# Kernel optimization log

Hardware: AMD Instinct MI355X
Metric: run time of the kernel (lower is better)

## Reference

```python
import jax, jax.numpy as jnp
import numpy as np
from jax import lax

B, T = 128, 128
MODEL = 128          # model_size = hidden_size = cell_size (w)
R = 4                # read heads
M = 64               # nr_cells
W = MODEL            # cell size
VOCAB = 512
CLIP = 20.0          # dnc default controller clip
DELTA = 1e-6         # dnc epsilon
IFACE = R * W + 3 * W + 5 * R + 3  # 919 interface outputs


def setup_inputs():
    key = jax.random.key(0)
    ks = jax.random.split(key, 12)
    g = lambda k, s, sc: jax.random.normal(k, s, dtype=jnp.float32) * sc
    H = MODEL
    return {
        'tokens': jax.random.randint(ks[0], (B, T), 0, VOCAB),
        'emb': g(ks[1], (VOCAB, MODEL), 0.02),
        # controller: 2-layer LSTM, layer0 input = model + r*w
        'w_ih0': g(ks[2], (4 * H, MODEL + R * W), 0.05),
        'w_hh0': g(ks[3], (4 * H, H), 0.05),
        'b_ih0': jnp.zeros((4 * H,), jnp.float32),
        'b_hh0': jnp.zeros((4 * H,), jnp.float32),
        'w_ih1': g(ks[4], (4 * H, H), 0.05),
        'w_hh1': g(ks[5], (4 * H, H), 0.05),
        'b_ih1': jnp.zeros((4 * H,), jnp.float32),
        'b_hh1': jnp.zeros((4 * H,), jnp.float32),
        # memory interface linear: hidden -> 919
        'w_iface': g(ks[6], (IFACE, H), 0.05),
        'b_iface': jnp.zeros((IFACE,), jnp.float32),
        # dnc output linear: (hidden + r*w) -> model
        'w_out': g(ks[7], (MODEL, H + R * W), 0.05),
        'b_out': jnp.zeros((MODEL,), jnp.float32),
        # DNCAE fc head: model -> vocab
        'w_fc': g(ks[8], (VOCAB, MODEL), 0.05),
        'b_fc': jnp.zeros((VOCAB,), jnp.float32),
        # dnc initializes controller h (and c = h.clone()) with xavier-uniform noise
        'h0': g(ks[9], (2, B, H), 0.1),
    }


def _lstm_step(x, h, c, w_ih, w_hh, b_ih, b_hh):
    gates = x @ w_ih.T + b_ih + h @ w_hh.T + b_hh
    i, f, g, o = jnp.split(gates, 4, axis=-1)  # pytorch gate order i,f,g,o
    c2 = jax.nn.sigmoid(f) * c + jax.nn.sigmoid(i) * jnp.tanh(g)
    h2 = jax.nn.sigmoid(o) * jnp.tanh(c2)
    return h2, c2


def _cosine(mem, keys):
    # mem (B,M,W), keys (B,K,W) -> similarity (B,K,M); dnc adds DELTA to norms
    mn = mem / (jnp.linalg.norm(mem, axis=2, keepdims=True) + DELTA)
    kn = keys / (jnp.linalg.norm(keys, axis=2, keepdims=True) + DELTA)
    return jnp.einsum('bmw,bkw->bkm', mn, kn)


def _dnc_forward(tokens, emb, w_ih0, w_hh0, b_ih0, b_hh0, w_ih1, w_hh1, b_ih1,
                 b_hh1, w_iface, b_iface, w_out, b_out, w_fc, b_fc, h0):
    x = emb[tokens]  # (B,T,MODEL)
    # ixaxaar dnc concatenates the *initial* last_read (zeros) to every timestep input
    xs = jnp.concatenate([x, jnp.zeros((B, T, R * W), x.dtype)], axis=-1)
    eye_mask = 1.0 - jnp.eye(M, dtype=x.dtype)

    def step(carry, x_t):
        hl0, hl1, cl0, cl1, mem, link, prec, rw, ww, usage = carry
        nh0, nc0 = _lstm_step(x_t, hl0, cl0, w_ih0, w_hh0, b_ih0, b_hh0)
        nh1, nc1 = _lstm_step(nh0, hl1, cl1, w_ih1, w_hh1, b_ih1, b_hh1)
        out = jnp.clip(nh1, -CLIP, CLIP)
        xi = out @ w_iface.T + b_iface  # (B, 919)
        o = R * W
        read_keys = jnp.tanh(xi[:, :R * W]).reshape(B, R, W)
        read_str = jax.nn.softplus(xi[:, o:o + R]); o += R
        write_key = jnp.tanh(xi[:, o:o + W]).reshape(B, 1, W); o += W
        write_str = jax.nn.softplus(xi[:, o:o + 1]); o += 1
        erase = jax.nn.sigmoid(xi[:, o:o + W]); o += W
        write_vec = jnp.tanh(xi[:, o:o + W]); o += W
        free_gates = jax.nn.sigmoid(xi[:, o:o + R]); o += R
        alloc_gate = jax.nn.sigmoid(xi[:, o:o + 1]); o += 1
        write_gate = jax.nn.sigmoid(xi[:, o:o + 1]); o += 1
        read_modes = jax.nn.softmax(xi[:, o:o + 3 * R].reshape(B, R, 3), axis=2)

        # ---- write phase ----
        # usage (single write head: 1-prod(1-ww) == ww)
        usage = usage + (1.0 - usage) * ww
        psi = jnp.prod(1.0 - free_gates[:, :, None] * rw, axis=1)  # (B,M)
        usage = usage * psi
        # content weighting on pre-write memory
        wcw = jax.nn.softmax(_cosine(mem, write_key) * write_str[:, :, None], axis=2)[:, 0, :]
        # allocation weighting via sorted-usage cumprod
        u = DELTA + (1.0 - DELTA) * usage
        phi = jnp.argsort(u, axis=1)
        sorted_u = jnp.take_along_axis(u, phi, axis=1)
        prod_su = jnp.cumprod(jnp.concatenate([jnp.ones((B, 1), u.dtype), sorted_u], axis=1), axis=1)[:, :-1]
        sorted_alloc = (1.0 - sorted_u) * prod_su
        alloc = jnp.take_along_axis(sorted_alloc, jnp.argsort(phi, axis=1), axis=1)
        # final write weighting (B,M)
        ww = write_gate * (alloc_gate * alloc + (1.0 - alloc_gate) * wcw)
        # erase + write memory
        mem = mem * (1.0 - ww[:, :, None] * erase[:, None, :]) + ww[:, :, None] * write_vec[:, None, :]
        # temporal link matrix
        ww_i = ww[:, :, None]
        ww_j = ww[:, None, :]
        link = (1.0 - ww_i - ww_j) * link + ww_i * prec[:, None, :]
        link = link * eye_mask
        prec = (1.0 - jnp.sum(ww, axis=1, keepdims=True)) * prec + ww

        # ---- read phase (on post-write memory) ----
        cw = jax.nn.softmax(_cosine(mem, read_keys) * read_str[:, :, None], axis=2)  # (B,R,M)
        fwd = jnp.einsum('bij,brj->bri', link, rw)
        bwd = jnp.einsum('bri,bij->brj', rw, link)
        rw = read_modes[:, :, 0:1] * bwd + read_modes[:, :, 1:2] * fwd + read_modes[:, :, 2:3] * cw
        read_vecs = jnp.einsum('brm,bmw->brw', rw, mem).reshape(B, R * W)

        y = jnp.concatenate([out, read_vecs], axis=-1) @ w_out.T + b_out  # (B,MODEL)
        return (nh0, nh1, nc0, nc1, mem, link, prec, rw, ww, usage), y

    z = jnp.zeros
    carry0 = (h0[0], h0[1], h0[0], h0[1],
              z((B, M, W), jnp.float32), z((B, M, M), jnp.float32), z((B, M), jnp.float32),
              z((B, R, M), jnp.float32), z((B, M), jnp.float32), z((B, M), jnp.float32))
    _, ys = lax.scan(step, carry0, jnp.swapaxes(xs, 0, 1))  # ys (T,B,MODEL)
    dnc_out = jnp.swapaxes(ys, 0, 1)  # (B,T,MODEL)
    logits = dnc_out @ w_fc.T + b_fc  # (B,T,VOCAB)
    return jnp.transpose(logits, (0, 2, 1))  # (B,VOCAB,T) like .permute(0,2,1)


def reference(tokens, emb, w_ih0, w_hh0, b_ih0, b_hh0, w_ih1, w_hh1, b_ih1,
              b_hh1, w_iface, b_iface, w_out, b_out, w_fc, b_fc, h0):
    return _dnc_forward(tokens, emb, w_ih0, w_hh0, b_ih0, b_hh0, w_ih1, w_hh1,
                        b_ih1, b_hh1, w_iface, b_iface, w_out, b_out, w_fc, b_fc, h0)
```

## Files before the change

### kernel.cpp

```cpp
#include <hip/hip_runtime.h>
#include <math.h>

#define B 128
#define T 128
#define H 128
#define RH 4
#define M 64
#define W 128
#define VOCAB 512
#define IFACE 919
#define G4 512
#define DELTA 1e-6f
#define CLIPV 20.0f

#define MEMLD 133
#define LNKLD 67
#define CH 8
#define XILD 928

__device__ __forceinline__ float sigmoidf_(float x){ return 1.0f/(1.0f+expf(-x)); }
__device__ __forceinline__ float softplusf_(float x){
  return fmaxf(x, 0.0f) + log1pf(expf(-fabsf(x)));
}
__device__ __forceinline__ float waveAllSum(float v){
  for (int off=1; off<64; off<<=1) v += __shfl_xor(v, off, 64);
  return v;
}
__device__ __forceinline__ float waveAllMax(float v){
  for (int off=1; off<64; off<<=1) v = fmaxf(v, __shfl_xor(v, off, 64));
  return v;
}

__global__ void k_transpose(const float* __restrict__ in, float* __restrict__ out,
                            int rows, int cols, int use_cols){
  int idx = blockIdx.x*blockDim.x + threadIdx.x;
  int total = rows*use_cols;
  if (idx < total){
    int r = idx / use_cols, c = idx - r*use_cols;
    out[c*rows + r] = in[r*cols + c];
  }
}

__global__ void k_xw0(const float* __restrict__ emb, const float* __restrict__ wih0T,
                      const float* __restrict__ b_ih0, const float* __restrict__ b_hh0,
                      float* __restrict__ xw0){
  __shared__ float e[H];
  int v = blockIdx.x, g = threadIdx.x;
  if (g < H) e[g] = emb[v*H + g];
  __syncthreads();
  float acc = b_ih0[g] + b_hh0[g];
  #pragma unroll 8
  for (int k=0;k<H;k++) acc += e[k]*wih0T[k*G4 + g];
  xw0[v*G4 + g] = acc;
}

__launch_bounds__(512, 1)
__global__ void k_tail(const float* __restrict__ stash, const float* __restrict__ w_out,
                       const float* __restrict__ b_out, const float* __restrict__ w_fc,
                       const float* __restrict__ b_fc, float* __restrict__ out){
  __shared__ __align__(16) float S[32*644];
  __shared__ float Y[32*129];
  const int tid = threadIdx.x;
  const long bt0 = (long)blockIdx.x*32;

  for (int idx = tid; idx < 32*640; idx += 512){
    int bt = idx / 640, k = idx - bt*640;
    S[bt*644 + k] = stash[(bt0+bt)*640 + k];
  }
  __syncthreads();
  {
    int og = tid >> 5, bt = tid & 31;
    const float4* s4 = (const float4*)(S + bt*644);
    #pragma unroll
    for (int oo = 0; oo < 8; ++oo){
      int o = og*8 + oo;
      const float4* w4 = (const float4*)(w_out + (size_t)o*640);
      float acc = b_out[o];
      #pragma unroll 8
      for (int k4 = 0; k4 < 160; ++k4){
        float4 w = w4[k4], s = s4[k4];
        acc += w.x*s.x + w.y*s.y + w.z*s.z + w.w*s.w;
      }
      Y[bt*129 + o] = acc;
    }
  }
  __syncthreads();
  {
    int t = tid & 31, vg = tid >> 5;
    int b  = (int)(bt0 >> 7);
    int tb = (int)(bt0 & 127);
    const float* yr = Y + t*129;
    #pragma unroll 2
    for (int vv = 0; vv < 32; ++vv){
      int v = vg*32 + vv;
      const float4* w4 = (const float4*)(w_fc + (size_t)v*H);
      float acc = b_fc[v];
      #pragma unroll 8
      for (int k4 = 0; k4 < 32; ++k4){
        float4 w = w4[k4];
        int k = k4*4;
        acc += w.x*yr[k] + w.y*yr[k+1] + w.z*yr[k+2] + w.w*yr[k+3];
      }
      out[((size_t)b*VOCAB + v)*T + tb + t] = acc;
    }
  }
}

__launch_bounds__(512, 1)
__global__ void k_dnc(const int* __restrict__ tokens,
                      const float* __restrict__ xw0,
                      const float* __restrict__ whh0T,
                      const float* __restrict__ w1catT,
                      const float* __restrict__ b_ih1,
                      const float* __restrict__ b_hh1,
                      const float* __restrict__ wifaceT,
                      const float* __restrict__ b_iface,
                      const float* __restrict__ h0,
                      float* __restrict__ xibuf,
                      float* __restrict__ stash,
                      unsigned* __restrict__ pflag,
                      unsigned* __restrict__ cflag)
{
  const int role = blockIdx.x >> 7;
  const int b = blockIdx.x & 127;
  const int tid = threadIdx.x;
  const int lane = tid & 63;
  const int wave = tid >> 6;

  __shared__ __align__(16) float hcat[2*H];
  __shared__ __align__(16) float c0s[H], c1s[H];
  __shared__ __align__(16) float mem[M*MEMLD];
  __shared__ float link[M*LNKLD];
  __shared__ float prec[M], ww[M], usage[M];
  __shared__ float rw[RH*M];
  __shared__ __align__(16) float gates[G4];
  __shared__ __align__(16) float rk[RH*W];
  __shared__ float wk[W], er[W], wv[W];
  __shared__ float memnorm[M];
  __shared__ float wcw[M], alloc_s[M];
  __shared__ float cwm[RH*M], fwd[RH*M], bwd[RH*M];
  __shared__ int   tok[T];
  __shared__ float rstr[RH], rmode[RH*3];
  __shared__ float s_wstr, s_ag, s_wg, s_wwsum, s_wkinv, s_rkinv[RH];
  __shared__ __align__(16) float xi_chunk[CH*XILD];
  __shared__ __align__(16) float out_s[CH*H];

  if (role == 0){
    const float b1sum = b_ih1[tid] + b_hh1[tid];
    const bool  two = (tid < IFACE-512);
    const float bi0 = b_iface[tid];
    const float bi1 = two ? b_iface[tid+512] : 0.f;

    if (tid < H){
      float hv0 = h0[0*B*H + b*H + tid];
      float hv1 = h0[1*B*H + b*H + tid];
      hcat[tid]=hv0; hcat[H+tid]=hv1; c0s[tid]=hv0; c1s[tid]=hv1;
    }
    if (tid < T) tok[tid] = tokens[b*T + tid];
    __syncthreads();

    for (int c = 0; c < T/CH; ++c){
      for (int s = 0; s < CH; ++s){
        const int t = c*CH + s;
        {
          float acc = xw0[(size_t)tok[t]*G4 + tid];
          const float* wp = whh0T + tid;
          #pragma unroll 8
          for (int k=0;k<H;k++) acc += hcat[k]*wp[k*G4];
          gates[tid] = acc;
        }
        __syncthreads();
        if (tid < H){
          float ig = sigmoidf_(gates[tid]);
          float ff = sigmoidf_(gates[H+tid]);
          float gg = tanhf(gates[2*H+tid]);
          float og = sigmoidf_(gates[3*H+tid]);
          float c2 = ff*c0s[tid] + ig*gg;
          c0s[tid] = c2;
          hcat[tid] = og*tanhf(c2);
        }
        __syncthreads();
        {
          float acc = b1sum;
          const float* wp1 = w1catT + tid;
          const float* wp2 = w1catT + 128*G4 + tid;
          #pragma unroll 4
          for (int k=0;k<H;k++) acc += hcat[k]*wp1[k*G4] + hcat[H+k]*wp2[k*G4];
          gates[tid] = acc;
        }
        __syncthreads();
        if (tid < H){
          float ig = sigmoidf_(gates[tid]);
          float ff = sigmoidf_(gates[H+tid]);
          float gg = tanhf(gates[2*H+tid]);
          float og = sigmoidf_(gates[3*H+tid]);
          float c2 = ff*c1s[tid] + ig*gg;
          c1s[tid] = c2;
          float h2 = og*tanhf(c2);
          hcat[H+tid] = h2;
          float ov = fminf(fmaxf(h2, -CLIPV), CLIPV);
          out_s[s*H + tid] = ov;
          stash[((long)b*T + t)*640 + tid] = ov;
        }
        __syncthreads();
      }

      if (c >= 2){
        if (tid == 0){
          while (__hip_atomic_load(&cflag[b], __ATOMIC_ACQUIRE,
                                   __HIP_MEMORY_SCOPE_AGENT) < (unsigned)(c-1))
            __builtin_amdgcn_s_sleep(2);
        }
        __syncthreads();
      }

      {
        float* xslot = xibuf + ((size_t)b*2 + (c&1))*(CH*XILD);
        float a0[CH], a1[CH];
        #pragma unroll
        for (int r=0;r<CH;r++){ a0[r] = bi0; a1[r] = bi1; }
        const float* wp1 = wifaceT + tid;
        const float* wp2 = wifaceT + tid + 512;
        #pragma unroll 4
        for (int k=0;k<H;k++){
          float w1 = wp1[k*IFACE];
          float w2 = two ? wp2[k*IFACE] : 0.f;
          #pragma unroll
          for (int r=0;r<CH;r++){
            float o = out_s[r*H + k];
            a0[r] += o*w1;
            a1[r] += o*w2;
          }
        }
        #pragma unroll
        for (int r=0;r<CH;r++){
          xslot[r*XILD + tid] = a0[r];
          if (two) xslot[r*XILD + tid + 512] = a1[r];
        }
      }
      __syncthreads();
      if (tid == 0)
        __hip_atomic_store(&pflag[b], (unsigned)(c+1),
                           __ATOMIC_RELEASE, __HIP_MEMORY_SCOPE_AGENT);
    }
  } else {
    for (int i = tid; i < M*MEMLD; i += 512) mem[i]=0.f;
    for (int i = tid; i < M*LNKLD; i += 512) link[i]=0.f;
    if (tid < M){ prec[tid]=0.f; ww[tid]=0.f; usage[tid]=0.f; }
    if (tid < RH*M) rw[tid]=0.f;
    __syncthreads();

    for (int c = 0; c < T/CH; ++c){
      if (tid == 0){
        while (__hip_atomic_load(&pflag[b], __ATOMIC_ACQUIRE,
                                 __HIP_MEMORY_SCOPE_AGENT) < (unsigned)(c+1))
          __builtin_amdgcn_s_sleep(4);
      }
      __syncthreads();

      {
        const float4* src = (const float4*)(xibuf + ((size_t)b*2 + (c&1))*(CH*XILD));
        float4* dst = (float4*)xi_chunk;
        for (int i = tid; i < CH*XILD/4; i += 512) dst[i] = src[i];
      }
      __syncthreads();
      if (tid == 0)
        __hip_atomic_store(&cflag[b], (unsigned)(c+1),
                           __ATOMIC_RELEASE, __HIP_MEMORY_SCOPE_AGENT);

      for (int s = 0; s < CH; ++s){
        const int t = c*CH + s;
        const long bt = (long)b*T + t;
        const float* xc = xi_chunk + s*XILD;

        rk[tid] = tanhf(xc[tid]);
        if (tid < W){
          wk[tid] = tanhf(xc[516+tid]);
          er[tid] = sigmoidf_(xc[645+tid]);
          wv[tid] = tanhf(xc[773+tid]);
        }
        if (tid < RH){
          rstr[tid] = softplusf_(xc[512+tid]);
          float a0 = xc[907+3*tid], a1 = xc[908+3*tid], a2 = xc[909+3*tid];
          float mx = fmaxf(a0, fmaxf(a1,a2));
          float e0=expf(a0-mx), e1=expf(a1-mx), e2=expf(a2-mx);
          float s3 = e0+e1+e2;
          rmode[3*tid]=e0/s3; rmode[3*tid+1]=e1/s3; rmode[3*tid+2]=e2/s3;
        }
        if (tid == 0){
          s_wstr = softplusf_(xc[644]);
          s_ag = sigmoidf_(xc[905]);
          s_wg = sigmoidf_(xc[906]);
        }
        if (tid < M){
          float f0 = sigmoidf_(xc[901]);
          float f1 = sigmoidf_(xc[902]);
          float f2 = sigmoidf_(xc[903]);
          float f3 = sigmoidf_(xc[904]);
          float um = usage[tid] + (1.0f-usage[tid])*ww[tid];
          float psi = (1.0f - f0*rw[tid])      * (1.0f - f1*rw[M+tid])
                    * (1.0f - f2*rw[2*M+tid])  * (1.0f - f3*rw[3*M+tid]);
          usage[tid] = um*psi;
        }
        {
          int row = tid >> 3, sub = tid & 7;
          float ss = 0.f;
          #pragma unroll
          for (int i=0;i<16;i++){ float v = mem[row*MEMLD + sub + 8*i]; ss += v*v; }
          ss += __shfl_down(ss,4,8); ss += __shfl_down(ss,2,8); ss += __shfl_down(ss,1,8);
          if (sub==0) memnorm[row] = 1.0f/(sqrtf(ss)+DELTA);
        }
        if (wave == 0){
          float v0 = tanhf(xc[516+lane]), v1 = tanhf(xc[516+lane+64]);
          float ss = waveAllSum(v0*v0+v1*v1);
          if (lane==0) s_wkinv = 1.0f/(sqrtf(ss)+DELTA);
        } else if (wave <= RH){
          int r = wave-1;
          float v0 = tanhf(xc[r*W+lane]), v1 = tanhf(xc[r*W+lane+64]);
          float ss = waveAllSum(v0*v0+v1*v1);
          if (lane==0) s_rkinv[r] = 1.0f/(sqrtf(ss)+DELTA);
        }
        __syncthreads();

        {
          int m = tid >> 3, sub = tid & 7;
          float d = 0.f;
          #pragma unroll
          for (int i=0;i<16;i++){ int e = sub + 8*i; d += mem[m*MEMLD + e]*wk[e]; }
          d += __shfl_down(d,4,8); d += __shfl_down(d,2,8); d += __shfl_down(d,1,8);
          if (sub==0) wcw[m] = d * memnorm[m] * s_wkinv * s_wstr;
        }
        __syncthreads();

        if (wave == 0){
          float x = wcw[lane];
          float mx = waveAllMax(x);
          float e = expf(x-mx);
          float s2 = waveAllSum(e);
          wcw[lane] = e/s2;
        } else if (wave == 1){
          float u = DELTA + (1.0f-DELTA)*usage[lane];
          int idx = lane;
          for (int k=2;k<=64;k<<=1){
            for (int j=k>>1;j>0;j>>=1){
              float ou = __shfl_xor(u, j, 64);
              int   oi = __shfl_xor(idx, j, 64);
              bool up = ((lane & k) == 0);
              bool iLower = ((lane & j) == 0);
              bool otherLess = (ou < u) || (ou == u && oi < idx);
              bool takeOther = (up == iLower) ? otherLess : !otherLess;
              if (takeOther){ u = ou; idx = oi; }
            }
          }
          float p = u;
          for (int d=1; d<64; d<<=1){
            float pv = __shfl_up(p, d, 64);
            if (lane >= d) p *= pv;
          }
          float ep = __shfl_up(p, 1, 64);
          if (lane == 0) ep = 1.0f;
          alloc_s[idx] = (1.0f - u) * ep;
        }
        __syncthreads();

        {
          const float cg = s_wg, ag = s_ag;
          #pragma unroll
          for (int e=0;e<16;e++){
            int f = tid + 512*e;
            int m = f >> 7, w = f & 127;
            float wwm = cg*(ag*alloc_s[m] + (1.0f-ag)*wcw[m]);
            mem[m*MEMLD+w] = mem[m*MEMLD+w]*(1.0f - wwm*er[w]) + wwm*wv[w];
          }
          #pragma unroll
          for (int e=0;e<8;e++){
            int f = tid + 512*e;
            int i = f >> 6, j = f & 63;
            float wwi = cg*(ag*alloc_s[i] + (1.0f-ag)*wcw[i]);
            float wwj = cg*(ag*alloc_s[j] + (1.0f-ag)*wcw[j]);
            float lv = (1.0f - wwi - wwj)*link[i*LNKLD+j] + wwi*prec[j];
            link[i*LNKLD+j] = (i==j) ? 0.0f : lv;
          }
          if (tid < M) ww[tid] = cg*(ag*alloc_s[tid] + (1.0f-ag)*wcw[tid]);
        }
        __syncthreads();

        {
          int row = tid >> 3, sub = tid & 7;
          float ss = 0.f;
          #pragma unroll
          for (int i=0;i<16;i++){ float v = mem[row*MEMLD + sub + 8*i]; ss += v*v; }
          ss += __shfl_down(ss,4,8); ss += __shfl_down(ss,2,8); ss += __shfl_down(ss,1,8);
          if (sub==0) memnorm[row] = 1.0f/(sqrtf(ss)+DELTA);
        }
        __syncthreads();

        {
          int r = tid >> 7, m = (tid >> 1) & 63, sub = tid & 1;
          float d = 0.f;
          #pragma unroll 8
          for (int i=0;i<64;i++){ int e = sub + 2*i; d += mem[m*MEMLD + e]*rk[r*W + e]; }
          d += __shfl_down(d,1,2);
          if (sub==0) cwm[r*M+m] = d * memnorm[m] * s_rkinv[r] * rstr[r];
        }
        if (tid < 256){
          int r = tid >> 6, i = tid & 63;
          float a = 0.f;
          #pragma unroll 8
          for (int j=0;j<M;j++) a += link[i*LNKLD+j]*rw[r*M+j];
          fwd[r*M+i] = a;
        } else {
          int q = tid - 256;
          int r = q >> 6, j = q & 63;
          float a = 0.f;
          #pragma unroll 8
          for (int i=0;i<M;i++) a += rw[r*M+i]*link[i*LNKLD+j];
          bwd[r*M+j] = a;
        }
        if (wave == 7){
          float s2 = waveAllSum(ww[lane]);
          if (lane==0) s_wwsum = s2;
        }
        __syncthreads();

        if (wave < RH){
          int r = wave;
          float x = cwm[r*M + lane];
          float mx = waveAllMax(x);
          float e = expf(x-mx);
          float s2 = waveAllSum(e);
          float cc = e/s2;
          rw[r*M+lane] = rmode[3*r]*bwd[r*M+lane] + rmode[3*r+1]*fwd[r*M+lane]
                       + rmode[3*r+2]*cc;
        } else if (wave == 4){
          prec[lane] = (1.0f - s_wwsum)*prec[lane] + ww[lane];
        }
        __syncthreads();

        {
          int r = tid >> 7, w = tid & 127;
          float a = 0.f;
          #pragma unroll 8
          for (int m=0;m<M;m++) a += rw[r*M+m]*mem[m*MEMLD+w];
          stash[bt*640 + 128 + tid] = a;
        }
        __syncthreads();
      }
    }
  }
}

extern "C" void kernel_launch(void* const* d_in, const int* in_sizes, int n_in,
                              void* d_out, int out_size, void* d_ws, size_t ws_size,
                              hipStream_t stream)
{
  const int*   tokens  = (const int*)d_in[0];
  const float* emb     = (const float*)d_in[1];
  const float* w_ih0   = (const float*)d_in[2];
  const float* w_hh0   = (const float*)d_in[3];
  const float* b_ih0   = (const float*)d_in[4];
  const float* b_hh0   = (const float*)d_in[5];
  const float* w_ih1   = (const float*)d_in[6];
  const float* w_hh1   = (const float*)d_in[7];
  const float* b_ih1   = (const float*)d_in[8];
  const float* b_hh1   = (const float*)d_in[9];
  const float* w_iface = (const float*)d_in[10];
  const float* b_iface = (const float*)d_in[11];
  const float* w_out   = (const float*)d_in[12];
  const float* b_out   = (const float*)d_in[13];
  const float* w_fc    = (const float*)d_in[14];
  const float* b_fc    = (const float*)d_in[15];
  const float* h0      = (const float*)d_in[16];
  float* out = (float*)d_out;
  float* ws  = (float*)d_ws;

  float* xw0     = ws;
  float* whh0T   = xw0     + 262144;
  float* w1catT  = whh0T   + 65536;
  float* wifaceT = w1catT  + 131072;
  float* wih0T   = wifaceT + 117632;
  float* stash   = wih0T   + 65536;
  float* xibuf   = stash   + 10485760;
  unsigned* pflag = (unsigned*)(xibuf + 1900544);
  unsigned* cflag = pflag + 128;

  auto tp = [&](const float* in, float* o, int rows, int cols, int use){
    int total = rows*use;
    k_transpose<<<(total+255)/256, 256, 0, stream>>>(in, o, rows, cols, use);
  };
  tp(w_ih0,   wih0T,          512, 640, 128);
  tp(w_hh0,   whh0T,          512, 128, 128);
  tp(w_ih1,   w1catT,         512, 128, 128);
  tp(w_hh1,   w1catT+128*G4,  512, 128, 128);
  tp(w_iface, wifaceT,        919, 128, 128);
  k_xw0<<<VOCAB, 512, 0, stream>>>(emb, wih0T, b_ih0, b_hh0, xw0);
  hipMemsetAsync(pflag, 0, 256*sizeof(unsigned), stream);
  k_dnc<<<2*B, 512, 0, stream>>>(tokens, xw0, whh0T, w1catT, b_ih1, b_hh1,
                                 wifaceT, b_iface, h0, xibuf, stash,
                                 pflag, cflag);
  k_tail<<<(B*T)/32, 512, 0, stream>>>(stash, w_out, b_out, w_fc, b_fc, out);
}
```

Before: 2.372 ms.

## Split interface projection between controller and memory roles, double chunk size

The 919-wide interface projection is split: the controller block computes the first 460 outputs and the memory block computes the remaining 459 from the stashed controller outputs after copying the chunk. The chunk size goes from 8 to 16 steps. This balances the two cooperating workgroups so the controller's critical path shortens, and it halves handshake frequency. The cost is extra work and a global reload of the stashed outputs on the memory side, plus larger register arrays and shared buffers.

```diff
diff --git a/kernel.cpp b/kernel.cpp
--- a/kernel.cpp
+++ b/kernel.cpp
@@ -15,8 +15,10 @@
 
 #define MEMLD 133
 #define LNKLD 67
-#define CH 8
+#define CH 16
 #define XILD 928
+#define PHALF 460
+#define XSLD 464
 
 __device__ __forceinline__ float sigmoidf_(float x){ return 1.0f/(1.0f+expf(-x)); }
 __device__ __forceinline__ float softplusf_(float x){
@@ -147,9 +149,7 @@
 
   if (role == 0){
     const float b1sum = b_ih1[tid] + b_hh1[tid];
-    const bool  two = (tid < IFACE-512);
-    const float bi0 = b_iface[tid];
-    const float bi1 = two ? b_iface[tid+512] : 0.f;
+    const float bif = (tid < PHALF) ? b_iface[tid] : 0.f;
 
     if (tid < H){
       float hv0 = h0[0*B*H + b*H + tid];
@@ -214,29 +214,20 @@
         __syncthreads();
       }
 
-      {
-        float* xslot = xibuf + ((size_t)b*2 + (c&1))*(CH*XILD);
-        float a0[CH], a1[CH];
+      if (tid < PHALF){
+        float* xslot = xibuf + ((size_t)b*2 + (c&1))*(CH*XSLD);
+        float a[CH];
         #pragma unroll
-        for (int r=0;r<CH;r++){ a0[r] = bi0; a1[r] = bi1; }
-        const float* wp1 = wifaceT + tid;
-        const float* wp2 = wifaceT + tid + 512;
+        for (int r=0;r<CH;r++) a[r] = bif;
+        const float* wp = wifaceT + tid;
         #pragma unroll 4
         for (int k=0;k<H;k++){
-          float w1 = wp1[k*IFACE];
-          float w2 = two ? wp2[k*IFACE] : 0.f;
-          #pragma unroll
-          for (int r=0;r<CH;r++){
-            float o = out_s[r*H + k];
-            a0[r] += o*w1;
-            a1[r] += o*w2;
-          }
+          float w1 = wp[k*IFACE];
+          #pragma unroll
+          for (int r=0;r<CH;r++) a[r] += out_s[r*H + k]*w1;
         }
         #pragma unroll
-        for (int r=0;r<CH;r++){
-          xslot[r*XILD + tid] = a0[r];
-          if (two) xslot[r*XILD + tid + 512] = a1[r];
-        }
+        for (int r=0;r<CH;r++) xslot[r*XSLD + tid] = a[r];
       }
       __syncthreads();
       if (tid == 0)
@@ -244,6 +235,8 @@
                            __ATOMIC_RELEASE, __HIP_MEMORY_SCOPE_AGENT);
     }
   } else {
+    const float bif2 = (tid < IFACE-PHALF) ? b_iface[PHALF+tid] : 0.f;
+
     for (int i = tid; i < M*MEMLD; i += 512) mem[i]=0.f;
     for (int i = tid; i < M*LNKLD; i += 512) link[i]=0.f;
     if (tid < M){ prec[tid]=0.f; ww[tid]=0.f; usage[tid]=0.f; }
@@ -258,15 +251,37 @@
       }
       __syncthreads();
 
+      for (int idx = tid; idx < CH*H; idx += 512){
+        int r = idx >> 7, k = idx & 127;
+        out_s[idx] = stash[((size_t)b*T + c*CH + r)*640 + k];
+      }
       {
-        const float4* src = (const float4*)(xibuf + ((size_t)b*2 + (c&1))*(CH*XILD));
-        float4* dst = (float4*)xi_chunk;
-        for (int i = tid; i < CH*XILD/4; i += 512) dst[i] = src[i];
+        const float* src = xibuf + ((size_t)b*2 + (c&1))*(CH*XSLD);
+        for (int idx = tid; idx < CH*(PHALF/4); idx += 512){
+          int r = idx / (PHALF/4), q = idx - r*(PHALF/4);
+          ((float4*)(xi_chunk + r*XILD))[q] = ((const float4*)(src + r*XSLD))[q];
+        }
       }
       __syncthreads();
       if (tid == 0)
         __hip_atomic_store(&cflag[b], (unsigned)(c+1),
                            __ATOMIC_RELEASE, __HIP_MEMORY_SCOPE_AGENT);
+
+      if (tid < IFACE-PHALF){
+        float a[CH];
+        #pragma unroll
+        for (int r=0;r<CH;r++) a[r] = bif2;
+        const float* wp = wifaceT + PHALF + tid;
+        #pragma unroll 4
+        for (int k=0;k<H;k++){
+          float w1 = wp[k*IFACE];
+          #pragma unroll
+          for (int r=0;r<CH;r++) a[r] += out_s[r*H + k]*w1;
+        }
+        #pragma unroll
+        for (int r=0;r<CH;r++) xi_chunk[r*XILD + PHALF + tid] = a[r];
+      }
+      __syncthreads();
 
       for (int s = 0; s < CH; ++s){
         const int t = c*CH + s;
```

Result: slower. 3.042 ms (+28.3%).
